# Kernel optimization log

Measured on AMD Instinct MI355X. Metric: run time of the kernel, lower is better.

Reference implementation:

```python
import jax, jax.numpy as jnp
import numpy as np
from jax import lax

B, T, N, D, H = 16, 64, 512, 8, 128
MID = 64  # MLP hidden


def _lstm_layer(x, Wih, Whh, bih, bhh):
    # x: [T, BN, Din]; weights per PyTorch layout: Wih [4H, Din], Whh [4H, H], gate order i,f,g,o
    BN = x.shape[1]
    h0 = jnp.zeros((BN, H), x.dtype)
    c0 = jnp.zeros((BN, H), x.dtype)
    b = bih + bhh

    def step(carry, xt):
        h, c = carry
        gates = xt @ Wih.T + h @ Whh.T + b  # [BN, 4H]
        i, f, g, o = jnp.split(gates, 4, axis=-1)
        i = jax.nn.sigmoid(i)
        f = jax.nn.sigmoid(f)
        g = jnp.tanh(g)
        o = jax.nn.sigmoid(o)
        c = f * c + i * g
        h = o * jnp.tanh(c)
        return (h, c), h

    (_, _), hs = lax.scan(step, (h0, c0), x)
    return hs  # [T, BN, H]


def setup_inputs() -> dict:
    key = jax.random.key(0)
    ks = jax.random.split(key, 20)
    s = 1.0 / np.sqrt(H)
    u = lambda k, shp: jax.random.uniform(k, shp, jnp.float32, -s, s)
    inp = {
        "in_tensor": jax.random.normal(ks[0], (B, T, N, D), jnp.float32),
        "Wih0": u(ks[1], (4 * H, D)),
        "Whh0": u(ks[2], (4 * H, H)),
        "bih0": u(ks[3], (4 * H,)),
        "bhh0": u(ks[4], (4 * H,)),
        "Wih1": u(ks[5], (4 * H, H)),
        "Whh1": u(ks[6], (4 * H, H)),
        "bih1": u(ks[7], (4 * H,)),
        "bhh1": u(ks[8], (4 * H,)),
        "mu_W1": u(ks[9], (MID, H)),
        "mu_b1": u(ks[10], (MID,)),
        "mu_W2": u(ks[11], (2, MID)),
        "mu_b2": u(ks[12], (2,)),
        "sg_W1": u(ks[13], (MID, H)),
        "sg_b1": u(ks[14], (MID,)),
        "sg_W2": u(ks[15], (2, MID)),
        "sg_b2": u(ks[16], (2,)),
    }
    return inp


def reference(in_tensor, Wih0, Whh0, bih0, bhh0, Wih1, Whh1, bih1, bhh1,
              mu_W1, mu_b1, mu_W2, mu_b2, sg_W1, sg_b1, sg_W2, sg_b2):
    # Batched equivalent of the per-sample loops: flatten (batch, node) -> BN
    x = jnp.transpose(in_tensor, (1, 0, 2, 3)).reshape(T, B * N, D)  # [T, BN, D]
    h1 = _lstm_layer(x, Wih0, Whh0, bih0, bhh0)
    h2 = _lstm_layer(h1, Wih1, Whh1, bih1, bhh1)
    last = h2[-1].reshape(B, N, H)  # last timestep, [B, N, H]
    mu = jax.nn.sigmoid((last @ mu_W1.T + mu_b1) @ mu_W2.T + mu_b2)          # [B, N, 2]
    sigma = jax.nn.sigmoid((last @ sg_W1.T + sg_b1) @ sg_W2.T + sg_b2) * 0.5  # [B, N, 2]
    return (mu, sigma)
```

## Files before the change

### kernel.cpp

```cpp
#include <hip/hip_runtime.h>
#include <hip/hip_bf16.h>

typedef unsigned short u16;
typedef unsigned int u32;
typedef __attribute__((ext_vector_type(8))) short bf16x8;
typedef __attribute__((ext_vector_type(4))) float f32x4;

#define T_STEPS 64
#define BN_TOT  8192
#define BM      32

#define OFF_WHH0  0u
#define OFF_WIH0  131072u
#define OFF_W1    163840u
#define OFF_B0    425984u
#define OFF_B1    428032u
#define OFF_WEFF  430080u
#define OFF_BEFF  432128u
#define OFF_XB    432192u

#define HB        8192
#define LDS_BYTES (131072 + 3*HB)

__device__ __forceinline__ u16 f2bu(float f) {
  unsigned u = __float_as_uint(f);
  unsigned r = (u + 0x7FFFu + ((u >> 16) & 1u)) >> 16;
  return (u16)r;
}
__device__ __forceinline__ float bu2f(u16 u) {
  return __uint_as_float(((unsigned)u) << 16);
}
__device__ __forceinline__ float fsig(float x) {
  return __builtin_amdgcn_rcpf(1.0f + __builtin_amdgcn_exp2f(-1.44269504f * x));
}
__device__ __forceinline__ unsigned cvt_pk_bf16(float lo, float hi) {
  unsigned r;
  asm("v_cvt_pk_bf16_f32 %0, %1, %2" : "=v"(r) : "v"(lo), "v"(hi));
  return r;
}
__device__ __forceinline__ f32x4 mfma16(bf16x8 a, bf16x8 b, f32x4 c) {
  return __builtin_amdgcn_mfma_f32_16x16x32_bf16(a, b, c, 0, 0, 0);
}

union U16x8 { u16 u[8]; uint4 q; };

__global__ void lstm_prep_w(const float* Wih0, const float* Whh0,
                            const float* bih0, const float* bhh0,
                            const float* Wih1, const float* Whh1,
                            const float* bih1, const float* bhh1,
                            const float* muW1, const float* mub1,
                            const float* muW2, const float* mub2,
                            const float* sgW1, const float* sgb1,
                            const float* sgW2, const float* sgb2,
                            unsigned char* ws)
{
  int id = blockIdx.x * 256 + threadIdx.x;
  u16* whh0_f = (u16*)(ws + OFF_WHH0);
  u16* wih0_f = (u16*)(ws + OFF_WIH0);
  u16* w1_f   = (u16*)(ws + OFF_W1);
  float* b0   = (float*)(ws + OFF_B0);
  float* b1   = (float*)(ws + OFF_B1);
  float* weff = (float*)(ws + OFF_WEFF);
  float* beff = (float*)(ws + OFF_BEFF);

  if (id < 8192) {
    int fid = id >> 6, lane = id & 63;
    int w = fid >> 4, g = (fid >> 2) & 3, kf = fid & 3;
    int r = g*128 + w*16 + (lane & 15);
    int k = kf*32 + (lane >> 4)*8;
    const float* src = Whh0 + r*128 + k;
    U16x8 t;
    #pragma unroll
    for (int i = 0; i < 8; ++i) t.u[i] = f2bu(src[i]);
    ((uint4*)whh0_f)[id] = t.q;
  } else if (id < 10240) {
    int c = id - 8192; int fid = c >> 6, lane = c & 63;
    int w = fid >> 2, g = fid & 3;
    U16x8 t;
    #pragma unroll
    for (int i = 0; i < 8; ++i) t.u[i] = 0;
    if (lane < 16) {
      int r = g*128 + w*16 + lane;
      #pragma unroll
      for (int i = 0; i < 8; ++i) t.u[i] = f2bu(Wih0[r*8 + i]);
    }
    ((uint4*)wih0_f)[c] = t.q;
  } else if (id < 26624) {
    int c = id - 10240; int fid = c >> 6, lane = c & 63;
    int w = fid >> 5, g = (fid >> 3) & 3, kf = fid & 7;
    int r = g*128 + w*16 + (lane & 15);
    int k = kf*32 + (lane >> 4)*8;
    const float* src = (k < 128) ? (Wih1 + r*128 + k) : (Whh1 + r*128 + (k-128));
    U16x8 t;
    #pragma unroll
    for (int i = 0; i < 8; ++i) t.u[i] = f2bu(src[i]);
    ((uint4*)w1_f)[c] = t.q;
  } else if (id < 27136) {
    int i = id - 26624; int w = i >> 6, g = (i >> 4) & 3, cc = i & 15;
    int r = g*128 + w*16 + cc;
    b0[i] = bih0[r] + bhh0[r];
  } else if (id < 27648) {
    int i = id - 27136; int w = i >> 6, g = (i >> 4) & 3, cc = i & 15;
    int r = g*128 + w*16 + cc;
    b1[i] = bih1[r] + bhh1[r];
  } else if (id < 28160) {
    int i = id - 27648; int o = i >> 7, k = i & 127;
    const float* W1p = (o < 2) ? muW1 : sgW1;
    const float* W2p = (o < 2) ? muW2 : sgW2;
    int oo = o & 1;
    float s = 0.f;
    for (int m = 0; m < 64; ++m) s += W2p[oo*64 + m] * W1p[m*128 + k];
    weff[i] = s;
  } else if (id < 28164) {
    int o = id - 28160; int oo = o & 1;
    const float* W2p = (o < 2) ? muW2 : sgW2;
    const float* b1p = (o < 2) ? mub1 : sgb1;
    const float* b2p = (o < 2) ? mub2 : sgb2;
    float s = b2p[oo];
    for (int m = 0; m < 64; ++m) s += W2p[oo*64 + m] * b1p[m];
    beff[o] = s;
  }
}

__global__ void lstm_prep_x(const float* in, unsigned char* ws)
{
  int id = blockIdx.x * 256 + threadIdx.x;
  if (id >= T_STEPS * BN_TOT) return;
  int t = id >> 13, s = id & 8191, b = s >> 9, n = s & 511;
  const float* src = in + (((b*64) + t)*512 + n)*8;
  U16x8 v;
  #pragma unroll
  for (int i = 0; i < 8; ++i) v.u[i] = f2bu(src[i]);
  *(uint4*)(ws + OFF_XB + (size_t)id * 16) = v.q;
}

#define ACT_BLOCK(ACC, CS, HBASE)                                          \
  { _Pragma("unroll")                                                      \
    for (int mf = 0; mf < 2; ++mf) {                                       \
      float hq[4];                                                         \
      _Pragma("unroll")                                                    \
      for (int q = 0; q < 4; ++q) {                                        \
        float ei = __builtin_amdgcn_exp2f(-1.44269504f * ACC[mf][0][q]);   \
        float ef = __builtin_amdgcn_exp2f(-1.44269504f * ACC[mf][1][q]);   \
        float eg = __builtin_amdgcn_exp2f(-2.88539008f * ACC[mf][2][q]);   \
        float eo = __builtin_amdgcn_exp2f(-1.44269504f * ACC[mf][3][q]);   \
        float a1 = 1.0f + ei, a2 = 1.0f + ef, a3 = 1.0f + eg;              \
        float p13 = a1 * a3;                                               \
        float num = fmaf(CS[mf][q], p13, (1.0f - eg) * a2);                \
        float c = num * __builtin_amdgcn_rcpf(p13 * a2);                   \
        CS[mf][q] = c;                                                     \
        float cc = fminf(fmaxf(c, -40.0f), 40.0f);                         \
        float ec = __builtin_amdgcn_exp2f(-2.88539008f * cc);              \
        hq[q] = (1.0f - ec) * __builtin_amdgcn_rcpf((1.0f + eo) * (1.0f + ec)); \
      }                                                                    \
      unsigned p01 = cvt_pk_bf16(hq[0], hq[1]);                            \
      unsigned p23 = cvt_pk_bf16(hq[2], hq[3]);                            \
      int rb = (mf*16 + lk*4);                                             \
      *(u16*)((HBASE) + wb + (rb  )*16) = (u16)p01;                        \
      *(u16*)((HBASE) + wb + (rb+1)*16) = (u16)(p01 >> 16);                \
      *(u16*)((HBASE) + wb + (rb+2)*16) = (u16)p23;                        \
      *(u16*)((HBASE) + wb + (rb+3)*16) = (u16)(p23 >> 16);                \
    } }

__global__ __launch_bounds__(512, 2) void lstm_fused(const unsigned char* ws, float* out)
{
  extern __shared__ unsigned char lds[];
  u16* whh0_lds = (u16*)lds;
  unsigned char* hA  = lds + 131072;
  unsigned char* hB0 = hA + HB;
  unsigned char* hB1 = hB0 + HB;

  const u16* whh0_f = (const u16*)(ws + OFF_WHH0);
  const u16* wih0_f = (const u16*)(ws + OFF_WIH0);
  const u16* w1_f   = (const u16*)(ws + OFF_W1);
  const float* b0a  = (const float*)(ws + OFF_B0);
  const float* b1a  = (const float*)(ws + OFF_B1);
  const float* weff = (const float*)(ws + OFF_WEFF);
  const float* beff = (const float*)(ws + OFF_BEFF);
  const u16* xb     = (const u16*)(ws + OFF_XB);

  const int tid = threadIdx.x;
  const int w = tid >> 6, l = tid & 63;
  const int lrow = l & 15, lk = l >> 4;
  const int s0 = blockIdx.x * BM;
  const int wb = (w*2 + (lrow >> 3))*512 + (lrow & 7)*2;

  for (int i = tid; i < 8192; i += 512)
    ((uint4*)whh0_lds)[i] = ((const uint4*)whh0_f)[i];
  for (int i = tid; i < 6144; i += 512) ((u32*)hA)[i] = 0;

  bf16x8 w1r[4][8];
  #pragma unroll
  for (int g = 0; g < 4; ++g)
    #pragma unroll
    for (int kf = 0; kf < 8; ++kf)
      w1r[g][kf] = *(const bf16x8*)(w1_f + ((((w*4+g)*8)+kf)*64 + l)*8);
  bf16x8 wih0r[4];
  #pragma unroll
  for (int g = 0; g < 4; ++g)
    wih0r[g] = *(const bf16x8*)(wih0_f + ((w*4+g)*64 + l)*8);
  float b0v[4], b1v[4];
  #pragma unroll
  for (int g = 0; g < 4; ++g) {
    b0v[g] = b0a[w*64 + g*16 + lrow];
    b1v[g] = b1a[w*64 + g*16 + lrow];
  }
  float c_a[2][4] = {{0,0,0,0},{0,0,0,0}};
  float c_b[2][4] = {{0,0,0,0},{0,0,0,0}};

  unsigned char* hbR = hB0;
  unsigned char* hbW = hB1;

  bf16x8 xf0 = {0,0,0,0,0,0,0,0}, xf1 = {0,0,0,0,0,0,0,0};
  if (lk == 0) {
    xf0 = *(const bf16x8*)(xb + (size_t)(s0 + lrow)*8);
    xf1 = *(const bf16x8*)(xb + (size_t)(s0 + 16 + lrow)*8);
  }
  __syncthreads();

  #pragma unroll 1
  for (int t = 0; t < T_STEPS; ++t) {
    f32x4 acc[2][4];
    #pragma unroll
    for (int g = 0; g < 4; ++g) {
      acc[0][g] = (f32x4){b0v[g], b0v[g], b0v[g], b0v[g]};
      acc[1][g] = (f32x4){b0v[g], b0v[g], b0v[g], b0v[g]};
    }
    #pragma unroll
    for (int g = 0; g < 4; ++g) {
      acc[0][g] = mfma16(xf0, wih0r[g], acc[0][g]);
      acc[1][g] = mfma16(xf1, wih0r[g], acc[1][g]);
    }
    if (t + 1 < T_STEPS && lk == 0) {
      xf0 = *(const bf16x8*)(xb + (size_t)((t+1)*8192 + s0 + lrow)*8);
      xf1 = *(const bf16x8*)(xb + (size_t)((t+1)*8192 + s0 + 16 + lrow)*8);
    }
    #pragma unroll
    for (int kf = 0; kf < 4; ++kf) {
      bf16x8 a0 = *(const bf16x8*)(hA + (kf*4 + lk)*512 + lrow*16);
      bf16x8 a1 = *(const bf16x8*)(hA + (kf*4 + lk)*512 + (16 + lrow)*16);
      #pragma unroll
      for (int g = 0; g < 4; ++g) {
        bf16x8 bfr = *(const bf16x8*)(whh0_lds + ((w*16 + g*4 + kf)*64 + l)*8);
        acc[0][g] = mfma16(a0, bfr, acc[0][g]);
        acc[1][g] = mfma16(a1, bfr, acc[1][g]);
      }
    }
    __syncthreads();
    ACT_BLOCK(acc, c_a, hA);
    __syncthreads();

    #pragma unroll
    for (int g = 0; g < 4; ++g) {
      acc[0][g] = (f32x4){b1v[g], b1v[g], b1v[g], b1v[g]};
      acc[1][g] = (f32x4){b1v[g], b1v[g], b1v[g], b1v[g]};
    }
    #pragma unroll
    for (int kf = 0; kf < 8; ++kf) {
      const unsigned char* hs = (kf < 4) ? hA : hbR;
      bf16x8 a0 = *(const bf16x8*)(hs + ((kf & 3)*4 + lk)*512 + lrow*16);
      bf16x8 a1 = *(const bf16x8*)(hs + ((kf & 3)*4 + lk)*512 + (16 + lrow)*16);
      #pragma unroll
      for (int g = 0; g < 4; ++g) {
        acc[0][g] = mfma16(a0, w1r[g][kf], acc[0][g]);
        acc[1][g] = mfma16(a1, w1r[g][kf], acc[1][g]);
      }
    }
    ACT_BLOCK(acc, c_b, hbW);
    { unsigned char* tp = hbR; hbR = hbW; hbW = tp; }
  }
  __syncthreads();

  if (tid < BM*4) {
    int m = tid >> 2, o = tid & 3;
    const float* wr = weff + o*128;
    float d = beff[o];
    #pragma unroll 4
    for (int kk = 0; kk < 16; ++kk) {
      bf16x8 hv = *(const bf16x8*)(hbR + kk*512 + m*16);
      #pragma unroll
      for (int j = 0; j < 8; ++j) d += bu2f((u16)hv[j]) * wr[kk*8 + j];
    }
    float v = fsig(d);
    if (o >= 2) v *= 0.5f;
    int s = s0 + m;
    out[(o >= 2 ? 16384 : 0) + s*2 + (o & 1)] = v;
  }
}

extern "C" void kernel_launch(void* const* d_in, const int* in_sizes, int n_in,
                              void* d_out, int out_size, void* d_ws, size_t ws_size,
                              hipStream_t stream) {
  (void)in_sizes; (void)n_in; (void)out_size; (void)ws_size;
  const float* in_tensor = (const float*)d_in[0];
  const float* Wih0 = (const float*)d_in[1];
  const float* Whh0 = (const float*)d_in[2];
  const float* bih0 = (const float*)d_in[3];
  const float* bhh0 = (const float*)d_in[4];
  const float* Wih1 = (const float*)d_in[5];
  const float* Whh1 = (const float*)d_in[6];
  const float* bih1 = (const float*)d_in[7];
  const float* bhh1 = (const float*)d_in[8];
  const float* muW1 = (const float*)d_in[9];
  const float* mub1 = (const float*)d_in[10];
  const float* muW2 = (const float*)d_in[11];
  const float* mub2 = (const float*)d_in[12];
  const float* sgW1 = (const float*)d_in[13];
  const float* sgb1 = (const float*)d_in[14];
  const float* sgW2 = (const float*)d_in[15];
  const float* sgb2 = (const float*)d_in[16];
  unsigned char* ws = (unsigned char*)d_ws;
  float* out = (float*)d_out;

  lstm_prep_w<<<dim3(111), dim3(256), 0, stream>>>(
      Wih0, Whh0, bih0, bhh0, Wih1, Whh1, bih1, bhh1,
      muW1, mub1, muW2, mub2, sgW1, sgb1, sgW2, sgb2, ws);
  lstm_prep_x<<<dim3(2048), dim3(256), 0, stream>>>(in_tensor, ws);

  (void)hipFuncSetAttribute((const void*)lstm_fused,
                            hipFuncAttributeMaxDynamicSharedMemorySize, LDS_BYTES);
  lstm_fused<<<dim3(256), dim3(512), LDS_BYTES, stream>>>(ws, out);
}
```

Baseline: 275.4 us.

## Skew LSTM layers across timesteps to cut one barrier per step

Software-pipelines the two LSTM layers so each iteration computes layer 1 for step t and layer 0 for step t+1, both reading from the same double-buffered hidden states. The layer-0 hidden buffer is now double-buffered too, adding 8 KB of LDS, so only one __syncthreads per timestep is needed instead of two. This gives the scheduler two independent MFMA chains to interleave. The x loads lose their lk==0 guard, and the extra LDS may affect occupancy at two blocks per CU.

```diff
diff --git a/kernel.cpp b/kernel.cpp
--- a/kernel.cpp
+++ b/kernel.cpp
@@ -20,7 +20,7 @@
 #define OFF_XB    432192u
 
 #define HB        8192
-#define LDS_BYTES (131072 + 3*HB)
+#define LDS_BYTES (131072 + 4*HB)
 
 __device__ __forceinline__ u16 f2bu(float f) {
   unsigned u = __float_as_uint(f);
@@ -166,8 +166,9 @@
 {
   extern __shared__ unsigned char lds[];
   u16* whh0_lds = (u16*)lds;
-  unsigned char* hA  = lds + 131072;
-  unsigned char* hB0 = hA + HB;
+  unsigned char* hA0 = lds + 131072;
+  unsigned char* hA1 = hA0 + HB;
+  unsigned char* hB0 = hA1 + HB;
   unsigned char* hB1 = hB0 + HB;
 
   const u16* whh0_f = (const u16*)(ws + OFF_WHH0);
@@ -187,7 +188,7 @@
 
   for (int i = tid; i < 8192; i += 512)
     ((uint4*)whh0_lds)[i] = ((const uint4*)whh0_f)[i];
-  for (int i = tid; i < 6144; i += 512) ((u32*)hA)[i] = 0;
+  for (int i = tid; i < 8192; i += 512) ((u32*)hA0)[i] = 0;
 
   bf16x8 w1r[4][8];
   #pragma unroll
@@ -208,66 +209,102 @@
   float c_a[2][4] = {{0,0,0,0},{0,0,0,0}};
   float c_b[2][4] = {{0,0,0,0},{0,0,0,0}};
 
-  unsigned char* hbR = hB0;
-  unsigned char* hbW = hB1;
-
-  bf16x8 xf0 = {0,0,0,0,0,0,0,0}, xf1 = {0,0,0,0,0,0,0,0};
-  if (lk == 0) {
-    xf0 = *(const bf16x8*)(xb + (size_t)(s0 + lrow)*8);
-    xf1 = *(const bf16x8*)(xb + (size_t)(s0 + 16 + lrow)*8);
-  }
+  unsigned char *aR = hA0, *aW = hA1, *bR = hB1, *bW = hB0;
+
   __syncthreads();
 
+  {
+    const u16* xrow = xb + (size_t)(s0 + lrow)*8;
+    bf16x8 xf0 = *(const bf16x8*)xrow;
+    bf16x8 xf1 = *(const bf16x8*)(xrow + 128);
+    f32x4 acc0[2][4];
+    #pragma unroll
+    for (int g = 0; g < 4; ++g) {
+      acc0[0][g] = (f32x4){b0v[g], b0v[g], b0v[g], b0v[g]};
+      acc0[1][g] = (f32x4){b0v[g], b0v[g], b0v[g], b0v[g]};
+    }
+    #pragma unroll
+    for (int g = 0; g < 4; ++g) {
+      acc0[0][g] = mfma16(xf0, wih0r[g], acc0[0][g]);
+      acc0[1][g] = mfma16(xf1, wih0r[g], acc0[1][g]);
+    }
+    ACT_BLOCK(acc0, c_a, aR);
+  }
+  __syncthreads();
+
   #pragma unroll 1
-  for (int t = 0; t < T_STEPS; ++t) {
-    f32x4 acc[2][4];
-    #pragma unroll
-    for (int g = 0; g < 4; ++g) {
-      acc[0][g] = (f32x4){b0v[g], b0v[g], b0v[g], b0v[g]};
-      acc[1][g] = (f32x4){b0v[g], b0v[g], b0v[g], b0v[g]};
-    }
-    #pragma unroll
-    for (int g = 0; g < 4; ++g) {
-      acc[0][g] = mfma16(xf0, wih0r[g], acc[0][g]);
-      acc[1][g] = mfma16(xf1, wih0r[g], acc[1][g]);
-    }
-    if (t + 1 < T_STEPS && lk == 0) {
-      xf0 = *(const bf16x8*)(xb + (size_t)((t+1)*8192 + s0 + lrow)*8);
-      xf1 = *(const bf16x8*)(xb + (size_t)((t+1)*8192 + s0 + 16 + lrow)*8);
+  for (int t = 0; t < T_STEPS - 1; ++t) {
+    f32x4 acc1[2][4];
+    #pragma unroll
+    for (int g = 0; g < 4; ++g) {
+      acc1[0][g] = (f32x4){b1v[g], b1v[g], b1v[g], b1v[g]};
+      acc1[1][g] = (f32x4){b1v[g], b1v[g], b1v[g], b1v[g]};
+    }
+    #pragma unroll
+    for (int kf = 0; kf < 8; ++kf) {
+      const unsigned char* hs = (kf < 4) ? aR : bR;
+      bf16x8 a0 = *(const bf16x8*)(hs + ((kf & 3)*4 + lk)*512 + lrow*16);
+      bf16x8 a1 = *(const bf16x8*)(hs + ((kf & 3)*4 + lk)*512 + (16 + lrow)*16);
+      #pragma unroll
+      for (int g = 0; g < 4; ++g) {
+        acc1[0][g] = mfma16(a0, w1r[g][kf], acc1[0][g]);
+        acc1[1][g] = mfma16(a1, w1r[g][kf], acc1[1][g]);
+      }
+    }
+    ACT_BLOCK(acc1, c_b, bW);
+
+    const u16* xrow = xb + (size_t)((t+1)*8192 + s0 + lrow)*8;
+    bf16x8 xf0 = *(const bf16x8*)xrow;
+    bf16x8 xf1 = *(const bf16x8*)(xrow + 128);
+
+    f32x4 acc0[2][4];
+    #pragma unroll
+    for (int g = 0; g < 4; ++g) {
+      acc0[0][g] = (f32x4){b0v[g], b0v[g], b0v[g], b0v[g]};
+      acc0[1][g] = (f32x4){b0v[g], b0v[g], b0v[g], b0v[g]};
+    }
+    #pragma unroll
+    for (int g = 0; g < 4; ++g) {
+      acc0[0][g] = mfma16(xf0, wih0r[g], acc0[0][g]);
+      acc0[1][g] = mfma16(xf1, wih0r[g], acc0[1][g]);
     }
     #pragma unroll
     for (int kf = 0; kf < 4; ++kf) {
-      bf16x8 a0 = *(const bf16x8*)(hA + (kf*4 + lk)*512 + lrow*16);
-      bf16x8 a1 = *(const bf16x8*)(hA + (kf*4 + lk)*512 + (16 + lrow)*16);
+      bf16x8 a0 = *(const bf16x8*)(aR + (kf*4 + lk)*512 + lrow*16);
+      bf16x8 a1 = *(const bf16x8*)(aR + (kf*4 + lk)*512 + (16 + lrow)*16);
       #pragma unroll
       for (int g = 0; g < 4; ++g) {
         bf16x8 bfr = *(const bf16x8*)(whh0_lds + ((w*16 + g*4 + kf)*64 + l)*8);
-        acc[0][g] = mfma16(a0, bfr, acc[0][g]);
-        acc[1][g] = mfma16(a1, bfr, acc[1][g]);
+        acc0[0][g] = mfma16(a0, bfr, acc0[0][g]);
+        acc0[1][g] = mfma16(a1, bfr, acc0[1][g]);
       }
     }
+    ACT_BLOCK(acc0, c_a, aW);
+
     __syncthreads();
-    ACT_BLOCK(acc, c_a, hA);
-    __syncthreads();
-
-    #pragma unroll
-    for (int g = 0; g < 4; ++g) {
-      acc[0][g] = (f32x4){b1v[g], b1v[g], b1v[g], b1v[g]};
-      acc[1][g] = (f32x4){b1v[g], b1v[g], b1v[g], b1v[g]};
+    { unsigned char* tp = aR; aR = aW; aW = tp; }
+    { unsigned char* tp = bR; bR = bW; bW = tp; }
+  }
+
+  {
+    f32x4 acc1[2][4];
+    #pragma unroll
+    for (int g = 0; g < 4; ++g) {
+      acc1[0][g] = (f32x4){b1v[g], b1v[g], b1v[g], b1v[g]};
+      acc1[1][g] = (f32x4){b1v[g], b1v[g], b1v[g], b1v[g]};
     }
     #pragma unroll
     for (int kf = 0; kf < 8; ++kf) {
-      const unsigned char* hs = (kf < 4) ? hA : hbR;
+      const unsigned char* hs = (kf < 4) ? aR : bR;
       bf16x8 a0 = *(const bf16x8*)(hs + ((kf & 3)*4 + lk)*512 + lrow*16);
       bf16x8 a1 = *(const bf16x8*)(hs + ((kf & 3)*4 + lk)*512 + (16 + lrow)*16);
       #pragma unroll
       for (int g = 0; g < 4; ++g) {
-        acc[0][g] = mfma16(a0, w1r[g][kf], acc[0][g]);
-        acc[1][g] = mfma16(a1, w1r[g][kf], acc[1][g]);
+        acc1[0][g] = mfma16(a0, w1r[g][kf], acc1[0][g]);
+        acc1[1][g] = mfma16(a1, w1r[g][kf], acc1[1][g]);
       }
     }
-    ACT_BLOCK(acc, c_b, hbW);
-    { unsigned char* tp = hbR; hbR = hbW; hbW = tp; }
+    ACT_BLOCK(acc1, c_b, bW);
   }
   __syncthreads();
 
@@ -277,7 +314,7 @@
     float d = beff[o];
     #pragma unroll 4
     for (int kk = 0; kk < 16; ++kk) {
-      bf16x8 hv = *(const bf16x8*)(hbR + kk*512 + m*16);
+      bf16x8 hv = *(const bf16x8*)(bW + kk*512 + m*16);
       #pragma unroll
       for (int j = 0; j < 8; ++j) d += bu2f((u16)hv[j]) * wr[kk*8 + j];
     }
```

Result: faster. 234.0 us (-15.0%).
